# Optimization experiments

Hardware: AMD Instinct MI355X
Metric: run time of the kernel (lower is better)

## Reference

```python
import jax, jax.numpy as jnp
import numpy as np

NCLASSES = 1000
K = 5
REG_STRENGTH = 1.0


def isotonic_l2(y):
    """Solve min_v 0.5||v - y||^2 s.t. v_1 >= v_2 >= ... >= v_n, per row.

    Uses the exact min-max characterization of isotonic regression:
      sol_i = min_{j<=i} max_{k>=i} mean(y[j..k])
    (equivalent to pool-adjacent-violators), fully vectorized.
    y: [B, n] -> [B, n]
    """
    b, n = y.shape
    cs = jnp.concatenate([jnp.zeros((b, 1), y.dtype), jnp.cumsum(y, axis=-1)], axis=-1)  # [B, n+1]
    j = jnp.arange(n)[:, None]  # block start
    k = jnp.arange(n)[None, :]  # block end
    length = (k - j + 1).astype(y.dtype)
    # M[b, j, k] = mean(y[b, j..k]) for k >= j, else -inf (ignored by the max)
    M = (cs[:, None, 1:] - cs[:, :-1, None]) / jnp.where(k >= j, length, 1.0)
    M = jnp.where(k >= j, M, -jnp.inf)
    A = jax.lax.cummax(M, axis=2, reverse=True)  # A[b, j, i] = max_{k>=i} M[b, j, k]
    A = jnp.where(j <= k, A, jnp.inf)            # restrict min to j <= i
    return jnp.min(A, axis=1)                     # [B, n]


def soft_rank(values, strength):
    """torchsort.soft_rank with l2 regularization.

    r = theta - sigma^{-1}(isotonic_l2(sort_desc(theta) - w)),  theta = values/strength,
    w = [n, n-1, ..., 1].  Larger values get larger (soft) ranks.
    """
    n = values.shape[-1]
    theta = values / strength
    perm = jnp.argsort(-theta, axis=-1)                 # descending order
    s = jnp.take_along_axis(theta, perm, axis=-1)
    inv_perm = jnp.argsort(perm, axis=-1)
    w = jnp.arange(n, 0, -1, dtype=values.dtype)
    sol = isotonic_l2(s - w[None, :])
    return jnp.take_along_axis(s - sol, inv_perm, axis=-1)


def setup_inputs() -> dict:
    key = jax.random.key(0)
    k1, k2 = jax.random.split(key)
    output = jax.random.normal(k1, (64, NCLASSES), dtype=jnp.float32)
    target = jax.random.randint(k2, (64,), 0, NCLASSES, dtype=jnp.int32)
    return {"output": output, "target": target}


def reference(output, target):
    ranks = soft_rank(output, REG_STRENGTH)                              # [B, n]
    ranks_label = jnp.take_along_axis(ranks, target[:, None], axis=-1)   # [B, 1]
    return jnp.mean(jax.nn.relu(NCLASSES - ranks_label - K + 1))
```

## Files before the change

### kernel.cpp

```cpp
#include <hip/hip_runtime.h>
#include <math.h>

#define N      1000
#define NTH2   256
#define MSLICE 16
#define SROW   1008
#define META   (64 * SROW)

__global__ __launch_bounds__(1024) void k1_sort_scan(
    const float* __restrict__ mat, const int* __restrict__ target,
    float* __restrict__ ws)
{
    __shared__ float sx[2][2][1024];
    __shared__ float wtot[2][8];
    __shared__ int   cnt_sh[2];

    const int tid  = threadIdx.x;
    const int h    = tid >> 9;
    const int t    = tid & 511;
    const int lane = tid & 63;
    const int w    = (tid >> 6) & 7;
    const int i0   = (w << 7) + lane;
    const int i1   = i0 + 64;
    const int r    = (blockIdx.x << 1) | h;
    const float* row = mat + r * N;
    const int   tgt  = target[r];
    const float tval = row[tgt];

    float r0 = row[i0];
    float r1 = (i1 < N) ? row[i1] : -INFINITY;
    if (t == 0) cnt_sh[h] = 0;

    int lc = ((r0 > tval) || (r0 == tval && i0 < tgt))
           + ((r1 > tval) || (r1 == tval && i1 < tgt));
    #pragma unroll
    for (int off = 32; off; off >>= 1) lc += __shfl_down(lc, off);
    __syncthreads();
    if (lane == 0 && lc) atomicAdd(&cnt_sh[h], lc);

    auto cas_shfl = [&](float& rr, int i, unsigned k, unsigned j) {
        float o = __shfl_xor(rr, (int)j);
        bool lower = ((lane & (int)j) == 0);
        bool desc  = ((i & (int)k) == 0);
        rr = (lower == desc) ? fmaxf(rr, o) : fminf(rr, o);
    };
    #pragma unroll
    for (unsigned k = 2; k <= 64; k <<= 1)
        #pragma unroll
        for (unsigned j = k >> 1; j; j >>= 1) { cas_shfl(r0, i0, k, j); cas_shfl(r1, i1, k, j); }
    int buf = 0;
    #pragma unroll
    for (unsigned k = 128; k <= 1024; k <<= 1) {
        #pragma unroll
        for (unsigned j = k >> 1; j >= 128; j >>= 1) {
            sx[h][buf][i0] = r0; sx[h][buf][i1] = r1;
            __syncthreads();
            float o0 = sx[h][buf][i0 ^ (int)j], o1 = sx[h][buf][i1 ^ (int)j];
            buf ^= 1;
            bool lower = ((i0 & (int)j) == 0);
            bool desc  = ((i0 & (int)k) == 0);
            r0 = (lower == desc) ? fmaxf(r0, o0) : fminf(r0, o0);
            r1 = (lower == desc) ? fmaxf(r1, o1) : fminf(r1, o1);
        }
        {
            bool desc = ((i0 & (int)k) == 0);
            float a = fmaxf(r0, r1), b = fminf(r0, r1);
            r0 = desc ? a : b;
            r1 = desc ? b : a;
        }
        #pragma unroll
        for (unsigned j = 32; j; j >>= 1) { cas_shfl(r0, i0, k, j); cas_shfl(r1, i1, k, j); }
    }

    if (i1 >= N) r1 = 0.0f;
    float incl0 = r0;
    #pragma unroll
    for (int off = 1; off < 64; off <<= 1) {
        float y = __shfl_up(incl0, off);
        if (lane >= off) incl0 += y;
    }
    float tot0 = __shfl(incl0, 63);
    float incl1 = r1;
    #pragma unroll
    for (int off = 1; off < 64; off <<= 1) {
        float y = __shfl_up(incl1, off);
        if (lane >= off) incl1 += y;
    }
    if (lane == 63) wtot[h][w] = incl0 + incl1;
    __syncthreads();
    float base = 0.0f;
    #pragma unroll
    for (int u = 0; u < 8; ++u) { float x = wtot[h][u]; if (u < w) base += x; }

    float* Sg = ws + r * SROW;
    if (t == 0) Sg[0] = 0.0f;
    Sg[i0 + 1] = base + incl0;
    if (i1 < N) Sg[i1 + 1] = base + tot0 + incl1;
    if (t == 0) {
        ((int*)ws)[META + r] = cnt_sh[h];
        ws[META + 64 + r]    = tval;
    }
}

__global__ __launch_bounds__(NTH2) void k2_minmax(
    const float* __restrict__ ws, float* __restrict__ mrs)
{
    __shared__ float Sloc[N];
    __shared__ float rtab[N];
    __shared__ float maxh[NTH2];

    const int r  = blockIdx.y;
    const int m  = blockIdx.x;
    const int t  = threadIdx.x;
    const int p  = ((const int*)ws)[META + r];
    const int j0 = m * 64;
    if (j0 > p) return;
    const int len = N - p;
    const float* Srow = ws + r * SROW;

    const int jl = t & 63;
    const int j  = j0 + jl;
    const float Sj = (j <= p) ? Srow[j] : 0.0f;

    for (int i = t; i < len; i += NTH2) Sloc[i] = Srow[p + 1 + i];
    for (int d = t; d < N; d += NTH2) rtab[d] = 1.0f / (float)(d + 1);
    __syncthreads();

    const int q  = t >> 6;
    const int k0 = (q * len) >> 2;
    const int k1 = ((q + 1) * len) >> 2;
    float maxv = -INFINITY;
    if (j <= p) {
        const float* sp = &Sloc[k0];
        const float* rp = &rtab[p + k0 - j];
        float c = 0.5f * (float)(j + p + k0) - (float)N;
        #pragma unroll 8
        for (int it = 0; it < k1 - k0; ++it) {
            float mval = fmaf(sp[it] - Sj, rp[it], c);
            maxv = fmaxf(maxv, mval);
            c += 0.5f;
        }
    }
    maxh[t] = maxv;
    __syncthreads();
    if (t < 64) {
        float mv = fmaxf(fmaxf(maxh[t], maxh[t + 64]),
                         fmaxf(maxh[t + 128], maxh[t + 192]));
        float minv = (j0 + t <= p) ? mv : INFINITY;
        #pragma unroll
        for (int off = 32; off; off >>= 1)
            minv = fminf(minv, __shfl_down(minv, off));
        if (t == 0) mrs[r * MSLICE + m] = minv;
    }
}

__global__ __launch_bounds__(64) void k3_loss(
    const float* __restrict__ ws, float* __restrict__ out, int nrows)
{
    const int t = threadIdx.x;
    float loss = 0.0f;
    if (t < nrows) {
        const int   p    = ((const int*)ws)[META + t];
        const float tval = ws[META + 64 + t];
        const float* slot = ws + META + 128 + t * MSLICE;
        const int nsl = (p >> 6) + 1;
        float sol = slot[0];
        for (int m = 1; m < nsl; ++m) sol = fminf(sol, slot[m]);
        loss = fmaxf(0.0f, (float)(N - 5 + 1) - (tval - sol));
    }
    #pragma unroll
    for (int off = 32; off; off >>= 1) loss += __shfl_down(loss, off);
    if (t == 0) out[0] = loss / (float)nrows;
}

__global__ __launch_bounds__(512) void topk_loss_mono(
    const float* __restrict__ mat, const int* __restrict__ target,
    float* __restrict__ d_out, int nrows)
{
    __shared__ float S[1025];
    __shared__ float rcp[N];
    __shared__ float sx[1024];
    __shared__ float wtot[8];
    __shared__ float red[8];
    __shared__ int   cnt_sh;

    const int tid  = threadIdx.x;
    const int lane = tid & 63;
    const int w    = tid >> 6;
    const int i0   = (w << 7) + lane;
    const int i1   = i0 + 64;
    const float* row = mat + blockIdx.x * N;
    const int   tgt  = target[blockIdx.x];
    const float tval = row[tgt];

    float r0 = row[i0];
    float r1 = (i1 < N) ? row[i1] : -INFINITY;
    if (tid == 0) cnt_sh = 0;
    rcp[tid] = 1.0f / (float)(tid + 1);
    if (tid + 512 < N) rcp[tid + 512] = 1.0f / (float)(tid + 512 + 1);

    int lc = ((r0 > tval) || (r0 == tval && i0 < tgt))
           + ((r1 > tval) || (r1 == tval && i1 < tgt));
    #pragma unroll
    for (int off = 32; off; off >>= 1) lc += __shfl_down(lc, off);
    __syncthreads();
    if (lane == 0 && lc) atomicAdd(&cnt_sh, lc);

    auto cas_shfl = [&](float& rr, int i, unsigned k, unsigned j) {
        float o = __shfl_xor(rr, (int)j);
        bool lower = ((lane & (int)j) == 0);
        bool desc  = ((i & (int)k) == 0);
        rr = (lower == desc) ? fmaxf(rr, o) : fminf(rr, o);
    };
    #pragma unroll
    for (unsigned k = 2; k <= 64; k <<= 1)
        #pragma unroll
        for (unsigned j = k >> 1; j; j >>= 1) { cas_shfl(r0, i0, k, j); cas_shfl(r1, i1, k, j); }
    #pragma unroll
    for (unsigned k = 128; k <= 1024; k <<= 1) {
        #pragma unroll
        for (unsigned j = k >> 1; j >= 128; j >>= 1) {
            __syncthreads();
            sx[i0] = r0; sx[i1] = r1;
            __syncthreads();
            float o0 = sx[i0 ^ (int)j], o1 = sx[i1 ^ (int)j];
            bool lower = ((i0 & (int)j) == 0);
            bool desc  = ((i0 & (int)k) == 0);
            r0 = (lower == desc) ? fmaxf(r0, o0) : fminf(r0, o0);
            r1 = (lower == desc) ? fmaxf(r1, o1) : fminf(r1, o1);
        }
        {
            bool desc = ((i0 & (int)k) == 0);
            float a = fmaxf(r0, r1), b = fminf(r0, r1);
            r0 = desc ? a : b;
            r1 = desc ? b : a;
        }
        #pragma unroll
        for (unsigned j = 32; j; j >>= 1) { cas_shfl(r0, i0, k, j); cas_shfl(r1, i1, k, j); }
    }

    if (i1 >= N) r1 = 0.0f;
    float incl0 = r0;
    #pragma unroll
    for (int off = 1; off < 64; off <<= 1) {
        float y = __shfl_up(incl0, off);
        if (lane >= off) incl0 += y;
    }
    float tot0 = __shfl(incl0, 63);
    float incl1 = r1;
    #pragma unroll
    for (int off = 1; off < 64; off <<= 1) {
        float y = __shfl_up(incl1, off);
        if (lane >= off) incl1 += y;
    }
    if (lane == 63) wtot[w] = incl0 + incl1;
    __syncthreads();
    float base = 0.0f;
    #pragma unroll
    for (int u = 0; u < 8; ++u) { float t = wtot[u]; if (u < w) base += t; }
    if (tid == 0) S[0] = 0.0f;
    S[i0 + 1] = base + incl0;
    S[i1 + 1] = base + tot0 + incl1;
    __syncthreads();

    const int p   = cnt_sh;
    const int len = N - p;
    float minv = INFINITY;
    for (int j = tid; j <= p; j += 512) {
        const float  Sj = S[j];
        const float* Sp = &S[p + 1];
        const float* rp = &rcp[p - j];
        const float  cj = 0.5f * (float)(j + p) - (float)N;
        float maxv = -INFINITY;
        #pragma unroll 8
        for (int it = 0; it < len; ++it) {
            float mm = fmaf(Sp[it] - Sj, rp[it], cj + 0.5f * (float)it);
            maxv = fmaxf(maxv, mm);
        }
        minv = fminf(minv, maxv);
    }
    #pragma unroll
    for (int off = 32; off; off >>= 1) minv = fminf(minv, __shfl_down(minv, off));
    if (lane == 0) red[w] = minv;
    __syncthreads();
    if (tid == 0) {
        float sol = red[0];
        #pragma unroll
        for (int u = 1; u < 8; ++u) sol = fminf(sol, red[u]);
        float rank_label = tval - sol;
        float loss = fmaxf(0.0f, (float)(N - 5 + 1) - rank_label);
        atomicAdd(d_out, loss / (float)nrows);
    }
}

extern "C" void kernel_launch(void* const* d_in, const int* in_sizes, int n_in,
                              void* d_out, int out_size, void* d_ws, size_t ws_size,
                              hipStream_t stream) {
    (void)n_in;
    const float* mat    = (const float*)d_in[0];
    const int*   target = (const int*)d_in[1];
    float*       out    = (float*)d_out;
    const int    nrows  = in_sizes[1];

    const size_t need = (size_t)(META + 128 + 64 * MSLICE) * sizeof(float);
    if (nrows == 64 && ws_size >= need) {
        float* ws  = (float*)d_ws;
        float* mrs = ws + META + 128;
        k1_sort_scan<<<nrows / 2, 1024, 0, stream>>>(mat, target, ws);
        dim3 g2(MSLICE, nrows);
        k2_minmax<<<g2, NTH2, 0, stream>>>(ws, mrs);
        k3_loss<<<1, 64, 0, stream>>>(ws, out, nrows);
    } else {
        hipMemsetAsync(out, 0, sizeof(float) * out_size, stream);
        topk_loss_mono<<<nrows, 512, 0, stream>>>(mat, target, out, nrows);
    }
}
```

Before: 71.48 us.

## Use one row per sort block and drop LDS staging in minmax kernel

The sort/scan kernel now runs one row per 512-thread block across 64 blocks, where before it packed two rows into 32 blocks of 1024 threads. The aim is to spread work over more CUs and to stop barriers from coupling two independent rows. The min-max kernel no longer copies the prefix sums and a reciprocal table into shared memory before a barrier. It reads prefix sums straight from global memory (cached) and computes 1/length with the hardware approximate reciprocal instruction. That removes the staging pass and the barrier, at the cost of global/L1 loads in the inner loop and reciprocal values that may differ slightly from exact division.

Measured after the change: 71.17 us. No clear change (-0.4%).

```diff
diff --git a/kernel.cpp b/kernel.cpp
--- a/kernel.cpp
+++ b/kernel.cpp
@@ -2,41 +2,40 @@
 #include <math.h>
 
 #define N      1000
+#define NTH1   512
 #define NTH2   256
 #define MSLICE 16
 #define SROW   1008
 #define META   (64 * SROW)
 
-__global__ __launch_bounds__(1024) void k1_sort_scan(
+__global__ __launch_bounds__(NTH1) void k1_sort_scan(
     const float* __restrict__ mat, const int* __restrict__ target,
     float* __restrict__ ws)
 {
-    __shared__ float sx[2][2][1024];
-    __shared__ float wtot[2][8];
-    __shared__ int   cnt_sh[2];
+    __shared__ float sx[2][1024];
+    __shared__ float wtot[8];
+    __shared__ int   cnt_sh;
 
     const int tid  = threadIdx.x;
-    const int h    = tid >> 9;
-    const int t    = tid & 511;
     const int lane = tid & 63;
-    const int w    = (tid >> 6) & 7;
+    const int w    = tid >> 6;
     const int i0   = (w << 7) + lane;
     const int i1   = i0 + 64;
-    const int r    = (blockIdx.x << 1) | h;
+    const int r    = blockIdx.x;
     const float* row = mat + r * N;
     const int   tgt  = target[r];
     const float tval = row[tgt];
 
     float r0 = row[i0];
     float r1 = (i1 < N) ? row[i1] : -INFINITY;
-    if (t == 0) cnt_sh[h] = 0;
+    if (tid == 0) cnt_sh = 0;
 
     int lc = ((r0 > tval) || (r0 == tval && i0 < tgt))
            + ((r1 > tval) || (r1 == tval && i1 < tgt));
     #pragma unroll
     for (int off = 32; off; off >>= 1) lc += __shfl_down(lc, off);
     __syncthreads();
-    if (lane == 0 && lc) atomicAdd(&cnt_sh[h], lc);
+    if (lane == 0 && lc) atomicAdd(&cnt_sh, lc);
 
     auto cas_shfl = [&](float& rr, int i, unsigned k, unsigned j) {
         float o = __shfl_xor(rr, (int)j);
@@ -53,9 +52,9 @@
     for (unsigned k = 128; k <= 1024; k <<= 1) {
         #pragma unroll
         for (unsigned j = k >> 1; j >= 128; j >>= 1) {
-            sx[h][buf][i0] = r0; sx[h][buf][i1] = r1;
+            sx[buf][i0] = r0; sx[buf][i1] = r1;
             __syncthreads();
-            float o0 = sx[h][buf][i0 ^ (int)j], o1 = sx[h][buf][i1 ^ (int)j];
+            float o0 = sx[buf][i0 ^ (int)j], o1 = sx[buf][i1 ^ (int)j];
             buf ^= 1;
             bool lower = ((i0 & (int)j) == 0);
             bool desc  = ((i0 & (int)k) == 0);
@@ -86,18 +85,18 @@
         float y = __shfl_up(incl1, off);
         if (lane >= off) incl1 += y;
     }
-    if (lane == 63) wtot[h][w] = incl0 + incl1;
+    if (lane == 63) wtot[w] = incl0 + incl1;
     __syncthreads();
     float base = 0.0f;
     #pragma unroll
-    for (int u = 0; u < 8; ++u) { float x = wtot[h][u]; if (u < w) base += x; }
+    for (int u = 0; u < 8; ++u) { float t = wtot[u]; if (u < w) base += t; }
 
     float* Sg = ws + r * SROW;
-    if (t == 0) Sg[0] = 0.0f;
+    if (tid == 0) Sg[0] = 0.0f;
     Sg[i0 + 1] = base + incl0;
     if (i1 < N) Sg[i1 + 1] = base + tot0 + incl1;
-    if (t == 0) {
-        ((int*)ws)[META + r] = cnt_sh[h];
+    if (tid == 0) {
+        ((int*)ws)[META + r] = cnt_sh;
         ws[META + 64 + r]    = tval;
     }
 }
@@ -105,14 +104,12 @@
 __global__ __launch_bounds__(NTH2) void k2_minmax(
     const float* __restrict__ ws, float* __restrict__ mrs)
 {
-    __shared__ float Sloc[N];
-    __shared__ float rtab[N];
     __shared__ float maxh[NTH2];
 
     const int r  = blockIdx.y;
     const int m  = blockIdx.x;
     const int t  = threadIdx.x;
-    const int p  = ((const int*)ws)[META + r];
+    const int p  = __builtin_amdgcn_readfirstlane(((const int*)ws)[META + r]);
     const int j0 = m * 64;
     if (j0 > p) return;
     const int len = N - p;
@@ -121,24 +118,22 @@
     const int jl = t & 63;
     const int j  = j0 + jl;
     const float Sj = (j <= p) ? Srow[j] : 0.0f;
-
-    for (int i = t; i < len; i += NTH2) Sloc[i] = Srow[p + 1 + i];
-    for (int d = t; d < N; d += NTH2) rtab[d] = 1.0f / (float)(d + 1);
-    __syncthreads();
 
     const int q  = t >> 6;
     const int k0 = (q * len) >> 2;
     const int k1 = ((q + 1) * len) >> 2;
     float maxv = -INFINITY;
     if (j <= p) {
-        const float* sp = &Sloc[k0];
-        const float* rp = &rtab[p + k0 - j];
-        float c = 0.5f * (float)(j + p + k0) - (float)N;
+        const float* su = Srow + p + 1 + k0;
+        float ld = (float)(p + k0 + 1 - j);
+        float c  = 0.5f * (float)(j + p + k0) - (float)N;
         #pragma unroll 8
         for (int it = 0; it < k1 - k0; ++it) {
-            float mval = fmaf(sp[it] - Sj, rp[it], c);
+            float rc   = __builtin_amdgcn_rcpf(ld);
+            float mval = fmaf(su[it] - Sj, rc, c);
             maxv = fmaxf(maxv, mval);
-            c += 0.5f;
+            ld += 1.0f;
+            c  += 0.5f;
         }
     }
     maxh[t] = maxv;
@@ -306,7 +301,7 @@
     if (nrows == 64 && ws_size >= need) {
         float* ws  = (float*)d_ws;
         float* mrs = ws + META + 128;
-        k1_sort_scan<<<nrows / 2, 1024, 0, stream>>>(mat, target, ws);
+        k1_sort_scan<<<nrows, NTH1, 0, stream>>>(mat, target, ws);
         dim3 g2(MSLICE, nrows);
         k2_minmax<<<g2, NTH2, 0, stream>>>(ws, mrs);
         k3_loss<<<1, 64, 0, stream>>>(ws, out, nrows);
```
